# Optimization experiments

Hardware: AMD Instinct MI355X
Metric: run time of the kernel (lower is better)

Reference implementation:

```python
import jax, jax.numpy as jnp
import numpy as np

B, N, L, D_MODEL, H, D_K, D_V = 8, 307, 64, 64, 4, 16, 16


def setup_inputs() -> dict:
    key = jax.random.key(0)
    ks = jax.random.split(key, 10)
    inp = {
        "input_Q": jax.random.normal(ks[0], (B, N, L, D_MODEL), jnp.float32),
        "input_K": jax.random.normal(ks[1], (B, N, L, D_MODEL), jnp.float32),
        "input_V": jax.random.normal(ks[2], (B, N, L, D_MODEL), jnp.float32),
        "attn_mask": jax.random.uniform(ks[3], (B, N, L, 1), jnp.float32),
        "res_att": jax.random.normal(ks[4], (B, N, H, L, L), jnp.float32),
        # Linear weights stored as [in, out] (torch nn.Linear weight transposed)
        "W_Q": jax.random.normal(ks[5], (D_MODEL, H * D_K), jnp.float32) / np.sqrt(D_MODEL),
        "W_K": jax.random.normal(ks[6], (D_MODEL, H * D_K), jnp.float32) / np.sqrt(D_MODEL),
        "W_V": jax.random.normal(ks[7], (D_MODEL, H * D_V), jnp.float32) / np.sqrt(D_MODEL),
        "W_fc": jax.random.normal(ks[8], (H * D_V, D_MODEL), jnp.float32) / np.sqrt(H * D_V),
        # freshly-constructed nn.LayerNorm has weight=1, bias=0
        "ln_scale": jnp.ones((D_MODEL,), jnp.float32),
        "ln_bias": jnp.zeros((D_MODEL,), jnp.float32),
    }
    return inp


def _layernorm(x, scale, bias, eps=1e-5):
    mu = jnp.mean(x, axis=-1, keepdims=True)
    var = jnp.mean(jnp.square(x - mu), axis=-1, keepdims=True)
    return (x - mu) * jax.lax.rsqrt(var + eps) * scale + bias


def reference(input_Q, input_K, input_V, attn_mask, res_att, W_Q, W_K, W_V, W_fc, ln_scale, ln_bias):
    # projections -> [B,N,H,L,d]
    def proj(x, W, d):
        y = jnp.einsum('bnlf,fe->bnle', x, W)
        return y.reshape(B, N, L, H, d).transpose(0, 1, 3, 2, 4)

    Q = proj(input_Q, W_Q, D_K)
    K = proj(input_K, W_K, D_K)
    V = proj(input_V, W_V, D_V)

    # scaled QK^T + residual attention bias: [B,N,H,Lq,Lk]
    scores = jnp.einsum('bnhqd,bnhkd->bnhqk', Q, K) / np.sqrt(D_K) + res_att
    # attn_mask [B,N,L,1] -> broadcast over heads (axis 2) and key dim (last)
    mask = attn_mask[:, :, None, :, :]  # [B,N,1,L,1]
    scores = jnp.where(mask > 0.5, jnp.float32(-1e9), scores)

    # NOTE: original softmaxes over dim=3 (the query axis), faithful here
    attn = jax.nn.softmax(scores, axis=3)
    context = jnp.einsum('bnhqk,bnhkd->bnhqd', attn, V)
    context = context.transpose(0, 1, 3, 2, 4).reshape(B, N, L, H * D_V)
    output = jnp.einsum('bnlc,cf->bnlf', context, W_fc)
    out = _layernorm(output + input_Q, ln_scale, ln_bias)
    return out, scores
```

## Files before the change

kernel.cpp:

```cpp
#include <hip/hip_runtime.h>

#define B_   8
#define N_   307
#define BN   (B_ * N_)
#define OUT_ELEMS (BN * 64 * 64)

typedef float f32x4 __attribute__((ext_vector_type(4)));
typedef short s16x8 __attribute__((ext_vector_type(8)));

__device__ __forceinline__ unsigned short f2bf(float x) {
    unsigned int u = __builtin_bit_cast(unsigned int, x);
    u += 0x7FFFu + ((u >> 16) & 1u);
    return (unsigned short)(u >> 16);
}

__device__ __forceinline__ int swz(int row) { return row ^ ((row >> 3) & 7); }

__device__ __forceinline__ s16x8 ldfrag(const unsigned short* p) {
    return *reinterpret_cast<const s16x8*>(p);
}

__device__ __forceinline__ s16x8 cvt8(float4 lo, float4 hi) {
    s16x8 f;
    f[0] = (short)f2bf(lo.x); f[1] = (short)f2bf(lo.y);
    f[2] = (short)f2bf(lo.z); f[3] = (short)f2bf(lo.w);
    f[4] = (short)f2bf(hi.x); f[5] = (short)f2bf(hi.y);
    f[6] = (short)f2bf(hi.z); f[7] = (short)f2bf(hi.w);
    return f;
}

__device__ __forceinline__ void stage_B(const float* __restrict__ src,
                                        unsigned short* dst, int tid) {
    const float4* s4 = reinterpret_cast<const float4*>(src);
#pragma unroll
    for (int i = 0; i < 4; ++i) {
        int idx = i * 256 + tid;
        float4 v = s4[idx];
        int k  = idx >> 4;
        int n0 = (idx & 15) << 2;
        int ki = k >> 5;
        int qd = (k >> 3) & 3;
        int j  = k & 7;
        float vv[4] = {v.x, v.y, v.z, v.w};
#pragma unroll
        for (int c = 0; c < 4; ++c) {
            int n = n0 + c;
            int row = ((n >> 4) * 2 + ki) * 64 + (qd << 4) + (n & 15);
            dst[(swz(row) << 3) + j] = f2bf(vv[c]);
        }
    }
}

__global__ __launch_bounds__(256, 4) void mta_kernel(
    const float* __restrict__ Xq, const float* __restrict__ Xk,
    const float* __restrict__ Xv, const float* __restrict__ maskp,
    const float* __restrict__ res, const float* __restrict__ Wq,
    const float* __restrict__ Wk, const float* __restrict__ Wv,
    const float* __restrict__ Wfc, const float* __restrict__ lnS,
    const float* __restrict__ lnB, float* __restrict__ out,
    float* __restrict__ scores_out)
{
    __shared__ __align__(16) unsigned char smem[32768];
    unsigned short* sKf = (unsigned short*)(smem);
    unsigned short* sQf = (unsigned short*)(smem + 8192);
    unsigned short* sVf = (unsigned short*)(smem + 16384);
    unsigned short* sWA = (unsigned short*)(smem + 24576);

    const int bn   = blockIdx.x;
    const int tid  = threadIdx.x;
    const int w    = tid >> 6;
    const int lane = tid & 63;
    const int quad = lane >> 4;
    const int l16  = lane & 15;
    const size_t base64 = (size_t)bn * 4096;

    const int toff = (w * 16 + quad * 4) * 64 + l16;

    float4 mv = *reinterpret_cast<const float4*>(maskp + bn * 64 + w * 16 + quad * 4);
    bool bm[4] = {mv.x > 0.5f, mv.y > 0.5f, mv.z > 0.5f, mv.w > 0.5f};

    float rA[4][4], rB[4][4];
    {
        const float* rp = res + (((size_t)(bn * 4)) << 12) + toff;
#pragma unroll
        for (int nt = 0; nt < 4; ++nt)
#pragma unroll
            for (int r = 0; r < 4; ++r)
                rA[nt][r] = rp[r * 64 + nt * 16];
    }

#pragma unroll 1
    for (int pj = 0; pj < 3; ++pj) {
        const float* Xs = (pj == 0) ? Xq : (pj == 1) ? Xk : Xv;
        const float* Ws = (pj == 0) ? Wq : (pj == 1) ? Wk : Wv;
        const float* p = Xs + base64 + (w * 16 + l16) * 64 + quad * 8;
        float4 x0 = *(const float4*)(p);      float4 x1 = *(const float4*)(p + 4);
        float4 x2 = *(const float4*)(p + 32); float4 x3 = *(const float4*)(p + 36);
        stage_B(Ws, sWA, tid);
        __syncthreads();
        s16x8 a0 = cvt8(x0, x1);
        s16x8 a1 = cvt8(x2, x3);
#pragma unroll
        for (int nt = 0; nt < 4; ++nt) {
            f32x4 acc = {0.f, 0.f, 0.f, 0.f};
            s16x8 b0 = ldfrag(sWA + (swz((nt * 2 + 0) * 64 + lane) << 3));
            s16x8 b1 = ldfrag(sWA + (swz((nt * 2 + 1) * 64 + lane) << 3));
            acc = __builtin_amdgcn_mfma_f32_16x16x32_bf16(a0, b0, acc, 0, 0, 0);
            acc = __builtin_amdgcn_mfma_f32_16x16x32_bf16(a1, b1, acc, 0, 0, 0);
            if (pj == 0) {
#pragma unroll
                for (int r = 0; r < 4; ++r) {
                    int rowq = (nt * 4 + w) * 32 + ((l16 >> 3) << 4) + quad * 4 + r;
                    sQf[(swz(rowq) << 3) + (l16 & 7)] = f2bf(acc[r] * 0.25f);
                }
            } else if (pj == 1) {
#pragma unroll
                for (int r = 0; r < 4; ++r) {
                    int rowk = (nt * 4 + w) * 32 + ((l16 >> 3) << 4) + quad * 4 + r;
                    sKf[(swz(rowk) << 3) + (l16 & 7)] = f2bf(acc[r]);
                }
            } else {
#pragma unroll
                for (int r = 0; r < 4; ++r) {
                    int kk = w * 16 + quad * 4 + r;
                    int rowv = (nt * 2 + (kk >> 5)) * 64 + (((kk >> 3) & 3) << 4) + l16;
                    sVf[(swz(rowv) << 3) + (kk & 7)] = f2bf(acc[r]);
                }
            }
        }
        __syncthreads();
    }

    f32x4 ctx[4];
#pragma unroll
    for (int h = 0; h < 4; ++h) ctx[h] = {0.f, 0.f, 0.f, 0.f};

    const s16x8 zf = {0, 0, 0, 0, 0, 0, 0, 0};
#pragma unroll
    for (int h = 0; h < 4; ++h) {
        const size_t sbase = ((size_t)(bn * 4 + h)) << 12;
        float (&rc)[4][4] = (h & 1) ? rB : rA;
        float (&rn)[4][4] = (h & 1) ? rA : rB;
        if (h < 3) {
            const float* rp = res + sbase + 4096 + toff;
#pragma unroll
            for (int nt = 0; nt < 4; ++nt)
#pragma unroll
                for (int r = 0; r < 4; ++r)
                    rn[nt][r] = rp[r * 64 + nt * 16];
        }

        s16x8 aq = zf;
        if (lane < 32) aq = ldfrag(sQf + (swz((h * 4 + w) * 32 + lane) << 3));
        float sv[4][4], Sw[4];
#pragma unroll
        for (int nt = 0; nt < 4; ++nt) {
            s16x8 bk = zf;
            if (lane < 32) bk = ldfrag(sKf + (swz((h * 4 + nt) * 32 + lane) << 3));
            f32x4 t = {0.f, 0.f, 0.f, 0.f};
            t = __builtin_amdgcn_mfma_f32_16x16x32_bf16(aq, bk, t, 0, 0, 0);
#pragma unroll
            for (int r = 0; r < 4; ++r) {
                float s = t[r] + rc[nt][r];
                s = bm[r] ? -1e9f : s;
                scores_out[sbase + toff + r * 64 + nt * 16] = s;
                sv[nt][r] = __expf(s);
            }
            float e = sv[nt][0] + sv[nt][1] + sv[nt][2] + sv[nt][3];
            e += __shfl_xor(e, 16, 64);
            e += __shfl_xor(e, 32, 64);
            Sw[nt] = e;
        }
        float* wS = (h == 0) ? (float*)(smem + 24576) : (float*)(smem + (h - 1) * 2048);
        if (quad == 0) {
#pragma unroll
            for (int nt = 0; nt < 4; ++nt) wS[(nt * 16 + l16) * 4 + w] = Sw[nt];
        }
        __syncthreads();

        float inv[4];
#pragma unroll
        for (int nt = 0; nt < 4; ++nt) {
            float4 vs = *reinterpret_cast<float4*>(&wS[(nt * 16 + l16) * 4]);
            inv[nt] = 1.0f / (vs.x + vs.y + vs.z + vs.w + 1e-30f);
        }
        if (h == 0) __syncthreads();

#pragma unroll
        for (int nt = 0; nt < 4; ++nt) {
            int k  = nt * 16 + l16;
            int rw = (w * 2 + (k >> 5)) * 64 + (((k >> 3) & 3) << 4) + quad * 4;
#pragma unroll
            for (int r = 0; r < 4; ++r)
                sWA[(swz(rw + r) << 3) + (k & 7)] = f2bf(sv[nt][r] * inv[nt]);
        }
        __syncthreads();

#pragma unroll
        for (int ki = 0; ki < 2; ++ki) {
            s16x8 ap = ldfrag(sWA + (swz((w * 2 + ki) * 64 + lane) << 3));
            s16x8 bv = ldfrag(sVf + (swz((h * 2 + ki) * 64 + lane) << 3));
            ctx[h] = __builtin_amdgcn_mfma_f32_16x16x32_bf16(ap, bv, ctx[h], 0, 0, 0);
        }
    }
    __syncthreads();

    float xres[4][4];
    {
        const float* xp = Xq + base64 + toff;
#pragma unroll
        for (int nt = 0; nt < 4; ++nt)
#pragma unroll
            for (int r = 0; r < 4; ++r)
                xres[nt][r] = xp[r * 64 + nt * 16];
    }
#pragma unroll
    for (int hh = 0; hh < 4; ++hh) {
        int c    = hh * 16 + l16;
        int rowb = (w * 2 + (c >> 5)) * 64 + (((c >> 3) & 3) << 4) + quad * 4;
#pragma unroll
        for (int r = 0; r < 4; ++r)
            sQf[(swz(rowb + r) << 3) + (c & 7)] = f2bf(ctx[hh][r]);
    }
    stage_B(Wfc, sWA, tid);
    __syncthreads();

    f32x4 oacc[4];
    {
        s16x8 a0 = ldfrag(sQf + (swz((w * 2 + 0) * 64 + lane) << 3));
        s16x8 a1 = ldfrag(sQf + (swz((w * 2 + 1) * 64 + lane) << 3));
#pragma unroll
        for (int nt = 0; nt < 4; ++nt) {
            f32x4 acc = {0.f, 0.f, 0.f, 0.f};
            s16x8 b0 = ldfrag(sWA + (swz((nt * 2 + 0) * 64 + lane) << 3));
            s16x8 b1 = ldfrag(sWA + (swz((nt * 2 + 1) * 64 + lane) << 3));
            acc = __builtin_amdgcn_mfma_f32_16x16x32_bf16(a0, b0, acc, 0, 0, 0);
            acc = __builtin_amdgcn_mfma_f32_16x16x32_bf16(a1, b1, acc, 0, 0, 0);
            oacc[nt] = acc;
        }
    }

    float scl[4], bia[4];
#pragma unroll
    for (int nt = 0; nt < 4; ++nt) {
        scl[nt] = lnS[nt * 16 + l16];
        bia[nt] = lnB[nt * 16 + l16];
    }
#pragma unroll
    for (int r = 0; r < 4; ++r) {
        float px[4], sum = 0.f, sq = 0.f;
#pragma unroll
        for (int nt = 0; nt < 4; ++nt) {
            float x = oacc[nt][r] + xres[nt][r];
            px[nt] = x; sum += x; sq += x * x;
        }
#pragma unroll
        for (int m = 1; m <= 8; m <<= 1) {
            sum += __shfl_xor(sum, m, 64);
            sq  += __shfl_xor(sq,  m, 64);
        }
        float mu   = sum * 0.015625f;
        float var  = sq * 0.015625f - mu * mu;
        float rstd = rsqrtf(var + 1e-5f);
#pragma unroll
        for (int nt = 0; nt < 4; ++nt) {
            out[base64 + toff + r * 64 + nt * 16] = (px[nt] - mu) * rstd * scl[nt] + bia[nt];
        }
    }
}

extern "C" void kernel_launch(void* const* d_in, const int* in_sizes, int n_in,
                              void* d_out, int out_size, void* d_ws, size_t ws_size,
                              hipStream_t stream) {
    const float* Xq   = (const float*)d_in[0];
    const float* Xk   = (const float*)d_in[1];
    const float* Xv   = (const float*)d_in[2];
    const float* msk  = (const float*)d_in[3];
    const float* res  = (const float*)d_in[4];
    const float* Wq   = (const float*)d_in[5];
    const float* Wk   = (const float*)d_in[6];
    const float* Wv   = (const float*)d_in[7];
    const float* Wfc  = (const float*)d_in[8];
    const float* lnS  = (const float*)d_in[9];
    const float* lnB  = (const float*)d_in[10];
    float* out    = (float*)d_out;
    float* scores = out + OUT_ELEMS;
    mta_kernel<<<BN, 256, 0, stream>>>(Xq, Xk, Xv, msk, res, Wq, Wk, Wv, Wfc,
                                       lnS, lnB, out, scores);
}
```

Before: 100.0 us.

## Assign one head per wave so softmax over queries needs no block sync

Attention work is redistributed so each of the four waves owns one head and computes the full 64x64 score tile for it. The query-axis softmax sum then stays inside a wave, using shuffles instead of shared-memory partial sums and several block barriers per head. The residual bias is loaded straight into the MFMA accumulators with double-buffered prefetch, and the Wfc staging is issued earlier. In exchange each wave holds more registers (eight accumulator tiles), which may lower occupancy, and it reuses the K/Q shared buffers as scratch for the probability tiles.

Result: slower. 121.3 us (+21.3%).

```diff
diff --git a/kernel.cpp b/kernel.cpp
--- a/kernel.cpp
+++ b/kernel.cpp
@@ -74,21 +74,6 @@
     const int l16  = lane & 15;
     const size_t base64 = (size_t)bn * 4096;
 
-    const int toff = (w * 16 + quad * 4) * 64 + l16;
-
-    float4 mv = *reinterpret_cast<const float4*>(maskp + bn * 64 + w * 16 + quad * 4);
-    bool bm[4] = {mv.x > 0.5f, mv.y > 0.5f, mv.z > 0.5f, mv.w > 0.5f};
-
-    float rA[4][4], rB[4][4];
-    {
-        const float* rp = res + (((size_t)(bn * 4)) << 12) + toff;
-#pragma unroll
-        for (int nt = 0; nt < 4; ++nt)
-#pragma unroll
-            for (int r = 0; r < 4; ++r)
-                rA[nt][r] = rp[r * 64 + nt * 16];
-    }
-
 #pragma unroll 1
     for (int pj = 0; pj < 3; ++pj) {
         const float* Xs = (pj == 0) ? Xq : (pj == 1) ? Xk : Xv;
@@ -131,80 +116,103 @@
         __syncthreads();
     }
 
+    stage_B(Wfc, sWA, tid);
+
+    const int h = w;
+    const size_t sbase = ((size_t)(bn * 4 + h)) << 12;
+
+    unsigned mbits = 0u;
+#pragma unroll
+    for (int mt = 0; mt < 4; ++mt) {
+        float4 mv = *reinterpret_cast<const float4*>(maskp + bn * 64 + mt * 16 + quad * 4);
+        mbits |= (mv.x > 0.5f ? 1u : 0u) << (mt * 4 + 0);
+        mbits |= (mv.y > 0.5f ? 1u : 0u) << (mt * 4 + 1);
+        mbits |= (mv.z > 0.5f ? 1u : 0u) << (mt * 4 + 2);
+        mbits |= (mv.w > 0.5f ? 1u : 0u) << (mt * 4 + 3);
+    }
+
+    const s16x8 zf = {0, 0, 0, 0, 0, 0, 0, 0};
+    s16x8 aq[4], bk[4];
+#pragma unroll
+    for (int t = 0; t < 4; ++t) {
+        aq[t] = (lane < 32) ? ldfrag(sQf + (swz((h * 4 + t) * 32 + lane) << 3)) : zf;
+        bk[t] = (lane < 32) ? ldfrag(sKf + (swz((h * 4 + t) * 32 + lane) << 3)) : zf;
+    }
+    unsigned short* scrA = sKf + w * 1024;
+    unsigned short* scrB = sQf + w * 1024;
+
+    const float* rp = res + sbase + quad * 256 + l16;
+    float*       sp = scores_out + sbase + quad * 256 + l16;
+
     f32x4 ctx[4];
 #pragma unroll
-    for (int h = 0; h < 4; ++h) ctx[h] = {0.f, 0.f, 0.f, 0.f};
-
-    const s16x8 zf = {0, 0, 0, 0, 0, 0, 0, 0};
-#pragma unroll
-    for (int h = 0; h < 4; ++h) {
-        const size_t sbase = ((size_t)(bn * 4 + h)) << 12;
-        float (&rc)[4][4] = (h & 1) ? rB : rA;
-        float (&rn)[4][4] = (h & 1) ? rA : rB;
-        if (h < 3) {
-            const float* rp = res + sbase + 4096 + toff;
-#pragma unroll
-            for (int nt = 0; nt < 4; ++nt)
+    for (int mt = 0; mt < 4; ++mt) ctx[mt] = {0.f, 0.f, 0.f, 0.f};
+
+    f32x4 acc[2][4];
+#pragma unroll
+    for (int mt = 0; mt < 4; ++mt)
+#pragma unroll
+        for (int r = 0; r < 4; ++r)
+            acc[0][mt][r] = rp[mt * 1024 + r * 64];
+
+#pragma unroll
+    for (int nt = 0; nt < 4; ++nt) {
+        const int cb = nt & 1, nb = cb ^ 1;
+#pragma unroll
+        for (int mt = 0; mt < 4; ++mt)
+            acc[cb][mt] = __builtin_amdgcn_mfma_f32_16x16x32_bf16(aq[mt], bk[nt], acc[cb][mt], 0, 0, 0);
+        if (nt < 3) {
+#pragma unroll
+            for (int mt = 0; mt < 4; ++mt)
 #pragma unroll
                 for (int r = 0; r < 4; ++r)
-                    rn[nt][r] = rp[r * 64 + nt * 16];
-        }
-
-        s16x8 aq = zf;
-        if (lane < 32) aq = ldfrag(sQf + (swz((h * 4 + w) * 32 + lane) << 3));
-        float sv[4][4], Sw[4];
-#pragma unroll
-        for (int nt = 0; nt < 4; ++nt) {
-            s16x8 bk = zf;
-            if (lane < 32) bk = ldfrag(sKf + (swz((h * 4 + nt) * 32 + lane) << 3));
-            f32x4 t = {0.f, 0.f, 0.f, 0.f};
-            t = __builtin_amdgcn_mfma_f32_16x16x32_bf16(aq, bk, t, 0, 0, 0);
+                    acc[nb][mt][r] = rp[mt * 1024 + r * 64 + (nt + 1) * 16];
+        }
+        float esum = 0.f;
+#pragma unroll
+        for (int mt = 0; mt < 4; ++mt)
 #pragma unroll
             for (int r = 0; r < 4; ++r) {
-                float s = t[r] + rc[nt][r];
-                s = bm[r] ? -1e9f : s;
-                scores_out[sbase + toff + r * 64 + nt * 16] = s;
-                sv[nt][r] = __expf(s);
+                float s = acc[cb][mt][r];
+                s = ((mbits >> (mt * 4 + r)) & 1u) ? -1e9f : s;
+                sp[mt * 1024 + r * 64 + nt * 16] = s;
+                float e = __expf(s);
+                acc[cb][mt][r] = e;
+                esum += e;
             }
-            float e = sv[nt][0] + sv[nt][1] + sv[nt][2] + sv[nt][3];
-            e += __shfl_xor(e, 16, 64);
-            e += __shfl_xor(e, 32, 64);
-            Sw[nt] = e;
-        }
-        float* wS = (h == 0) ? (float*)(smem + 24576) : (float*)(smem + (h - 1) * 2048);
-        if (quad == 0) {
-#pragma unroll
-            for (int nt = 0; nt < 4; ++nt) wS[(nt * 16 + l16) * 4 + w] = Sw[nt];
-        }
-        __syncthreads();
-
-        float inv[4];
-#pragma unroll
-        for (int nt = 0; nt < 4; ++nt) {
-            float4 vs = *reinterpret_cast<float4*>(&wS[(nt * 16 + l16) * 4]);
-            inv[nt] = 1.0f / (vs.x + vs.y + vs.z + vs.w + 1e-30f);
-        }
-        if (h == 0) __syncthreads();
-
-#pragma unroll
-        for (int nt = 0; nt < 4; ++nt) {
-            int k  = nt * 16 + l16;
-            int rw = (w * 2 + (k >> 5)) * 64 + (((k >> 3) & 3) << 4) + quad * 4;
+        esum += __shfl_xor(esum, 16, 64);
+        esum += __shfl_xor(esum, 32, 64);
+        float inv = 1.0f / (esum + 1e-30f);
+#pragma unroll
+        for (int mt = 0; mt < 4; ++mt) {
+            unsigned short* scr = ((mt < 2) ? scrA : scrB) + (mt & 1) * 512;
+            int rl = (((nt * 2 + (l16 >> 3)) & 3) << 4) + quad * 4;
 #pragma unroll
             for (int r = 0; r < 4; ++r)
-                sWA[(swz(rw + r) << 3) + (k & 7)] = f2bf(sv[nt][r] * inv[nt]);
-        }
-        __syncthreads();
-
-#pragma unroll
-        for (int ki = 0; ki < 2; ++ki) {
-            s16x8 ap = ldfrag(sWA + (swz((w * 2 + ki) * 64 + lane) << 3));
+                scr[(swz(rl + r) << 3) + (l16 & 7)] = f2bf(acc[cb][mt][r] * inv);
+        }
+        if (cb == 1) {
+            const int ki = nt >> 1;
             s16x8 bv = ldfrag(sVf + (swz((h * 2 + ki) * 64 + lane) << 3));
-            ctx[h] = __builtin_amdgcn_mfma_f32_16x16x32_bf16(ap, bv, ctx[h], 0, 0, 0);
-        }
-    }
+#pragma unroll
+            for (int mt = 0; mt < 4; ++mt) {
+                s16x8 ap = ldfrag(((mt < 2) ? scrA : scrB) + (mt & 1) * 512 + (swz(lane) << 3));
+                ctx[mt] = __builtin_amdgcn_mfma_f32_16x16x32_bf16(ap, bv, ctx[mt], 0, 0, 0);
+            }
+        }
+    }
+
     __syncthreads();
 
+#pragma unroll
+    for (int mt = 0; mt < 4; ++mt) {
+        int c    = h * 16 + l16;
+        int rowb = (mt * 2 + (c >> 5)) * 64 + (((c >> 3) & 3) << 4) + quad * 4;
+#pragma unroll
+        for (int r = 0; r < 4; ++r)
+            sQf[(swz(rowb + r) << 3) + (c & 7)] = f2bf(ctx[mt][r]);
+    }
+    const int toff = (w * 16 + quad * 4) * 64 + l16;
     float xres[4][4];
     {
         const float* xp = Xq + base64 + toff;
@@ -214,15 +222,12 @@
             for (int r = 0; r < 4; ++r)
                 xres[nt][r] = xp[r * 64 + nt * 16];
     }
-#pragma unroll
-    for (int hh = 0; hh < 4; ++hh) {
-        int c    = hh * 16 + l16;
-        int rowb = (w * 2 + (c >> 5)) * 64 + (((c >> 3) & 3) << 4) + quad * 4;
-#pragma unroll
-        for (int r = 0; r < 4; ++r)
-            sQf[(swz(rowb + r) << 3) + (c & 7)] = f2bf(ctx[hh][r]);
-    }
-    stage_B(Wfc, sWA, tid);
+    float scl[4], bia[4];
+#pragma unroll
+    for (int nt = 0; nt < 4; ++nt) {
+        scl[nt] = lnS[nt * 16 + l16];
+        bia[nt] = lnB[nt * 16 + l16];
+    }
     __syncthreads();
 
     f32x4 oacc[4];
@@ -231,21 +236,15 @@
         s16x8 a1 = ldfrag(sQf + (swz((w * 2 + 1) * 64 + lane) << 3));
 #pragma unroll
         for (int nt = 0; nt < 4; ++nt) {
-            f32x4 acc = {0.f, 0.f, 0.f, 0.f};
+            f32x4 a = {0.f, 0.f, 0.f, 0.f};
             s16x8 b0 = ldfrag(sWA + (swz((nt * 2 + 0) * 64 + lane) << 3));
             s16x8 b1 = ldfrag(sWA + (swz((nt * 2 + 1) * 64 + lane) << 3));
-            acc = __builtin_amdgcn_mfma_f32_16x16x32_bf16(a0, b0, acc, 0, 0, 0);
-            acc = __builtin_amdgcn_mfma_f32_16x16x32_bf16(a1, b1, acc, 0, 0, 0);
-            oacc[nt] = acc;
-        }
-    }
-
-    float scl[4], bia[4];
-#pragma unroll
-    for (int nt = 0; nt < 4; ++nt) {
-        scl[nt] = lnS[nt * 16 + l16];
-        bia[nt] = lnB[nt * 16 + l16];
-    }
+            a = __builtin_amdgcn_mfma_f32_16x16x32_bf16(a0, b0, a, 0, 0, 0);
+            a = __builtin_amdgcn_mfma_f32_16x16x32_bf16(a1, b1, a, 0, 0, 0);
+            oacc[nt] = a;
+        }
+    }
+
 #pragma unroll
     for (int r = 0; r < 4; ++r) {
         float px[4], sum = 0.f, sq = 0.f;
```

## Keep Q in registers via transposed MFMA, shrink LDS, fold residual into accumulator

Applied to the files above, without the earlier changes.

Computes the Q projection with swapped MFMA operands so the packed bf16 Q fragments stay in registers and are redistributed with shuffles, which removes the 8KB Q shared buffer. Shared memory drops to 24KB and the launch bound rises to 6 blocks per CU to raise occupancy. The residual attention bias is passed in as the MFMA accumulator, one barrier inside the head loop is removed, and the Xq residual and LayerNorm parameter loads are moved into the last head iteration. The higher block target risks register spills, and removing the barrier between the sWA probability writes and the cross-wave reads may introduce a race.

Measured after the change: 249.2 us. +149.2%, slower.

```diff
diff --git a/kernel.cpp b/kernel.cpp
--- a/kernel.cpp
+++ b/kernel.cpp
@@ -7,6 +7,7 @@
 
 typedef float f32x4 __attribute__((ext_vector_type(4)));
 typedef short s16x8 __attribute__((ext_vector_type(8)));
+typedef unsigned int u32x4 __attribute__((ext_vector_type(4)));
 
 __device__ __forceinline__ unsigned short f2bf(float x) {
     unsigned int u = __builtin_bit_cast(unsigned int, x);
@@ -51,7 +52,7 @@
     }
 }
 
-__global__ __launch_bounds__(256, 4) void mta_kernel(
+__global__ __launch_bounds__(256, 6) void mta_kernel(
     const float* __restrict__ Xq, const float* __restrict__ Xk,
     const float* __restrict__ Xv, const float* __restrict__ maskp,
     const float* __restrict__ res, const float* __restrict__ Wq,
@@ -60,11 +61,10 @@
     const float* __restrict__ lnB, float* __restrict__ out,
     float* __restrict__ scores_out)
 {
-    __shared__ __align__(16) unsigned char smem[32768];
+    __shared__ __align__(16) unsigned char smem[24576];
     unsigned short* sKf = (unsigned short*)(smem);
-    unsigned short* sQf = (unsigned short*)(smem + 8192);
-    unsigned short* sVf = (unsigned short*)(smem + 16384);
-    unsigned short* sWA = (unsigned short*)(smem + 24576);
+    unsigned short* sVf = (unsigned short*)(smem + 8192);
+    unsigned short* sWA = (unsigned short*)(smem + 16384);
 
     const int bn   = blockIdx.x;
     const int tid  = threadIdx.x;
@@ -88,6 +88,8 @@
             for (int r = 0; r < 4; ++r)
                 rA[nt][r] = rp[r * 64 + nt * 16];
     }
+
+    unsigned qpk[4][2];
 
 #pragma unroll 1
     for (int pj = 0; pj < 3; ++pj) {
@@ -105,26 +107,29 @@
             f32x4 acc = {0.f, 0.f, 0.f, 0.f};
             s16x8 b0 = ldfrag(sWA + (swz((nt * 2 + 0) * 64 + lane) << 3));
             s16x8 b1 = ldfrag(sWA + (swz((nt * 2 + 1) * 64 + lane) << 3));
-            acc = __builtin_amdgcn_mfma_f32_16x16x32_bf16(a0, b0, acc, 0, 0, 0);
-            acc = __builtin_amdgcn_mfma_f32_16x16x32_bf16(a1, b1, acc, 0, 0, 0);
             if (pj == 0) {
-#pragma unroll
-                for (int r = 0; r < 4; ++r) {
-                    int rowq = (nt * 4 + w) * 32 + ((l16 >> 3) << 4) + quad * 4 + r;
-                    sQf[(swz(rowq) << 3) + (l16 & 7)] = f2bf(acc[r] * 0.25f);
-                }
-            } else if (pj == 1) {
-#pragma unroll
-                for (int r = 0; r < 4; ++r) {
-                    int rowk = (nt * 4 + w) * 32 + ((l16 >> 3) << 4) + quad * 4 + r;
-                    sKf[(swz(rowk) << 3) + (l16 & 7)] = f2bf(acc[r]);
-                }
+                acc = __builtin_amdgcn_mfma_f32_16x16x32_bf16(b0, a0, acc, 0, 0, 0);
+                acc = __builtin_amdgcn_mfma_f32_16x16x32_bf16(b1, a1, acc, 0, 0, 0);
+                qpk[nt][0] = (unsigned)f2bf(acc[0] * 0.25f)
+                           | ((unsigned)f2bf(acc[1] * 0.25f) << 16);
+                qpk[nt][1] = (unsigned)f2bf(acc[2] * 0.25f)
+                           | ((unsigned)f2bf(acc[3] * 0.25f) << 16);
             } else {
-#pragma unroll
-                for (int r = 0; r < 4; ++r) {
-                    int kk = w * 16 + quad * 4 + r;
-                    int rowv = (nt * 2 + (kk >> 5)) * 64 + (((kk >> 3) & 3) << 4) + l16;
-                    sVf[(swz(rowv) << 3) + (kk & 7)] = f2bf(acc[r]);
+                acc = __builtin_amdgcn_mfma_f32_16x16x32_bf16(a0, b0, acc, 0, 0, 0);
+                acc = __builtin_amdgcn_mfma_f32_16x16x32_bf16(a1, b1, acc, 0, 0, 0);
+                if (pj == 1) {
+#pragma unroll
+                    for (int r = 0; r < 4; ++r) {
+                        int rowk = (nt * 4 + w) * 32 + ((l16 >> 3) << 4) + quad * 4 + r;
+                        sKf[(swz(rowk) << 3) + (l16 & 7)] = f2bf(acc[r]);
+                    }
+                } else {
+#pragma unroll
+                    for (int r = 0; r < 4; ++r) {
+                        int kk = w * 16 + quad * 4 + r;
+                        int rowv = (nt * 2 + (kk >> 5)) * 64 + (((kk >> 3) & 3) << 4) + l16;
+                        sVf[(swz(rowv) << 3) + (kk & 7)] = f2bf(acc[r]);
+                    }
                 }
             }
         }
@@ -134,6 +139,8 @@
     f32x4 ctx[4];
 #pragma unroll
     for (int h = 0; h < 4; ++h) ctx[h] = {0.f, 0.f, 0.f, 0.f};
+
+    float xres[4][4], scl[4], bia[4];
 
     const s16x8 zf = {0, 0, 0, 0, 0, 0, 0, 0};
 #pragma unroll
@@ -148,21 +155,39 @@
 #pragma unroll
                 for (int r = 0; r < 4; ++r)
                     rn[nt][r] = rp[r * 64 + nt * 16];
-        }
-
-        s16x8 aq = zf;
-        if (lane < 32) aq = ldfrag(sQf + (swz((h * 4 + w) * 32 + lane) << 3));
+        } else {
+            const float* xp = Xq + base64 + toff;
+#pragma unroll
+            for (int nt = 0; nt < 4; ++nt) {
+#pragma unroll
+                for (int r = 0; r < 4; ++r) xres[nt][r] = xp[r * 64 + nt * 16];
+                scl[nt] = lnS[nt * 16 + l16];
+                bia[nt] = lnB[nt * 16 + l16];
+            }
+        }
+
+        s16x8 aq;
+        {
+            int p0 = ((lane & 16) << 1) + l16;
+            unsigned w0 = __shfl(qpk[h][0], p0, 64);
+            unsigned w1 = __shfl(qpk[h][1], p0, 64);
+            unsigned w2 = __shfl(qpk[h][0], p0 + 16, 64);
+            unsigned w3 = __shfl(qpk[h][1], p0 + 16, 64);
+            if (lane >= 32) { w0 = 0; w1 = 0; w2 = 0; w3 = 0; }
+            u32x4 uv = {w0, w1, w2, w3};
+            aq = __builtin_bit_cast(s16x8, uv);
+        }
+
         float sv[4][4], Sw[4];
 #pragma unroll
         for (int nt = 0; nt < 4; ++nt) {
             s16x8 bk = zf;
             if (lane < 32) bk = ldfrag(sKf + (swz((h * 4 + nt) * 32 + lane) << 3));
-            f32x4 t = {0.f, 0.f, 0.f, 0.f};
-            t = __builtin_amdgcn_mfma_f32_16x16x32_bf16(aq, bk, t, 0, 0, 0);
+            f32x4 cin = {rc[nt][0], rc[nt][1], rc[nt][2], rc[nt][3]};
+            f32x4 t = __builtin_amdgcn_mfma_f32_16x16x32_bf16(aq, bk, cin, 0, 0, 0);
 #pragma unroll
             for (int r = 0; r < 4; ++r) {
-                float s = t[r] + rc[nt][r];
-                s = bm[r] ? -1e9f : s;
+                float s = bm[r] ? -1e9f : t[r];
                 scores_out[sbase + toff + r * 64 + nt * 16] = s;
                 sv[nt][r] = __expf(s);
             }
@@ -171,7 +196,7 @@
             e += __shfl_xor(e, 32, 64);
             Sw[nt] = e;
         }
-        float* wS = (h == 0) ? (float*)(smem + 24576) : (float*)(smem + (h - 1) * 2048);
+        float* wS = (h == 0) ? (float*)(smem + 16384) : (float*)(smem + (h - 1) * 2048);
         if (quad == 0) {
 #pragma unroll
             for (int nt = 0; nt < 4; ++nt) wS[(nt * 16 + l16) * 4 + w] = Sw[nt];
@@ -182,7 +207,7 @@
 #pragma unroll
         for (int nt = 0; nt < 4; ++nt) {
             float4 vs = *reinterpret_cast<float4*>(&wS[(nt * 16 + l16) * 4]);
-            inv[nt] = 1.0f / (vs.x + vs.y + vs.z + vs.w + 1e-30f);
+            inv[nt] = 1.0f / (vs.x + vs.y + vs.z + vs.w);
         }
         if (h == 0) __syncthreads();
 
@@ -194,8 +219,6 @@
             for (int r = 0; r < 4; ++r)
                 sWA[(swz(rw + r) << 3) + (k & 7)] = f2bf(sv[nt][r] * inv[nt]);
         }
-        __syncthreads();
-
 #pragma unroll
         for (int ki = 0; ki < 2; ++ki) {
             s16x8 ap = ldfrag(sWA + (swz((w * 2 + ki) * 64 + lane) << 3));
@@ -205,47 +228,32 @@
     }
     __syncthreads();
 
-    float xres[4][4];
-    {
-        const float* xp = Xq + base64 + toff;
-#pragma unroll
-        for (int nt = 0; nt < 4; ++nt)
-#pragma unroll
-            for (int r = 0; r < 4; ++r)
-                xres[nt][r] = xp[r * 64 + nt * 16];
-    }
 #pragma unroll
     for (int hh = 0; hh < 4; ++hh) {
         int c    = hh * 16 + l16;
         int rowb = (w * 2 + (c >> 5)) * 64 + (((c >> 3) & 3) << 4) + quad * 4;
 #pragma unroll
         for (int r = 0; r < 4; ++r)
-            sQf[(swz(rowb + r) << 3) + (c & 7)] = f2bf(ctx[hh][r]);
+            sKf[(swz(rowb + r) << 3) + (c & 7)] = f2bf(ctx[hh][r]);
     }
     stage_B(Wfc, sWA, tid);
     __syncthreads();
 
     f32x4 oacc[4];
     {
-        s16x8 a0 = ldfrag(sQf + (swz((w * 2 + 0) * 64 + lane) << 3));
-        s16x8 a1 = ldfrag(sQf + (swz((w * 2 + 1) * 64 + lane) << 3));
-#pragma unroll
-        for (int nt = 0; nt < 4; ++nt) {
-            f32x4 acc = {0.f, 0.f, 0.f, 0.f};
+        s16x8 a0 = ldfrag(sKf + (swz((w * 2 + 0) * 64 + lane) << 3));
+        s16x8 a1 = ldfrag(sKf + (swz((w * 2 + 1) * 64 + lane) << 3));
+#pragma unroll
+        for (int nt = 0; nt < 4; ++nt) {
+            f32x4 a = {0.f, 0.f, 0.f, 0.f};
             s16x8 b0 = ldfrag(sWA + (swz((nt * 2 + 0) * 64 + lane) << 3));
             s16x8 b1 = ldfrag(sWA + (swz((nt * 2 + 1) * 64 + lane) << 3));
-            acc = __builtin_amdgcn_mfma_f32_16x16x32_bf16(a0, b0, acc, 0, 0, 0);
-            acc = __builtin_amdgcn_mfma_f32_16x16x32_bf16(a1, b1, acc, 0, 0, 0);
-            oacc[nt] = acc;
-        }
-    }
-
-    float scl[4], bia[4];
-#pragma unroll
-    for (int nt = 0; nt < 4; ++nt) {
-        scl[nt] = lnS[nt * 16 + l16];
-        bia[nt] = lnB[nt * 16 + l16];
-    }
+            a = __builtin_amdgcn_mfma_f32_16x16x32_bf16(a0, b0, a, 0, 0, 0);
+            a = __builtin_amdgcn_mfma_f32_16x16x32_bf16(a1, b1, a, 0, 0, 0);
+            oacc[nt] = a;
+        }
+    }
+
 #pragma unroll
     for (int r = 0; r < 4; ++r) {
         float px[4], sum = 0.f, sq = 0.f;
```

## Transpose score tiles so softmax reduces in-wave and use double-buffered P

Applied to the files above, without the earlier changes.

Swaps the MFMA operands for QK^T so each wave holds full query columns for its keys. The query-axis softmax sum then reduces with intra-wave shuffles instead of a cross-wave shared-memory exchange and an extra barrier. The residual bias is fed as the MFMA accumulator, and res and score accesses become contiguous 16-byte vector loads and stores. The probability tile is double-buffered across heads to drop a barrier, at the cost of 8KB more LDS per block and recomputing exp twice.

Result: slower. 103.1 us (+3.1%).

```diff
diff --git a/kernel.cpp b/kernel.cpp
--- a/kernel.cpp
+++ b/kernel.cpp
@@ -60,11 +60,12 @@
     const float* __restrict__ lnB, float* __restrict__ out,
     float* __restrict__ scores_out)
 {
-    __shared__ __align__(16) unsigned char smem[32768];
+    __shared__ __align__(16) unsigned char smem[40960];
     unsigned short* sKf = (unsigned short*)(smem);
     unsigned short* sQf = (unsigned short*)(smem + 8192);
     unsigned short* sVf = (unsigned short*)(smem + 16384);
-    unsigned short* sWA = (unsigned short*)(smem + 24576);
+    unsigned short* sW0 = (unsigned short*)(smem + 24576);
+    unsigned short* sW1 = (unsigned short*)(smem + 32768);
 
     const int bn   = blockIdx.x;
     const int tid  = threadIdx.x;
@@ -74,19 +75,19 @@
     const int l16  = lane & 15;
     const size_t base64 = (size_t)bn * 4096;
 
-    const int toff = (w * 16 + quad * 4) * 64 + l16;
-
-    float4 mv = *reinterpret_cast<const float4*>(maskp + bn * 64 + w * 16 + quad * 4);
-    bool bm[4] = {mv.x > 0.5f, mv.y > 0.5f, mv.z > 0.5f, mv.w > 0.5f};
-
-    float rA[4][4], rB[4][4];
+    const int soff0 = l16 * 64 + w * 16 + quad * 4;
+
+    bool bmv[4];
+#pragma unroll
+    for (int nt = 0; nt < 4; ++nt)
+        bmv[nt] = maskp[bn * 64 + nt * 16 + l16] > 0.5f;
+
+    f32x4 rA[4];
     {
-        const float* rp = res + (((size_t)(bn * 4)) << 12) + toff;
+        const float* rp = res + (((size_t)(bn * 4)) << 12) + soff0;
 #pragma unroll
         for (int nt = 0; nt < 4; ++nt)
-#pragma unroll
-            for (int r = 0; r < 4; ++r)
-                rA[nt][r] = rp[r * 64 + nt * 16];
+            rA[nt] = *reinterpret_cast<const f32x4*>(rp + nt * 1024);
     }
 
 #pragma unroll 1
@@ -96,15 +97,15 @@
         const float* p = Xs + base64 + (w * 16 + l16) * 64 + quad * 8;
         float4 x0 = *(const float4*)(p);      float4 x1 = *(const float4*)(p + 4);
         float4 x2 = *(const float4*)(p + 32); float4 x3 = *(const float4*)(p + 36);
-        stage_B(Ws, sWA, tid);
+        stage_B(Ws, sW0, tid);
         __syncthreads();
         s16x8 a0 = cvt8(x0, x1);
         s16x8 a1 = cvt8(x2, x3);
 #pragma unroll
         for (int nt = 0; nt < 4; ++nt) {
             f32x4 acc = {0.f, 0.f, 0.f, 0.f};
-            s16x8 b0 = ldfrag(sWA + (swz((nt * 2 + 0) * 64 + lane) << 3));
-            s16x8 b1 = ldfrag(sWA + (swz((nt * 2 + 1) * 64 + lane) << 3));
+            s16x8 b0 = ldfrag(sW0 + (swz((nt * 2 + 0) * 64 + lane) << 3));
+            s16x8 b1 = ldfrag(sW0 + (swz((nt * 2 + 1) * 64 + lane) << 3));
             acc = __builtin_amdgcn_mfma_f32_16x16x32_bf16(a0, b0, acc, 0, 0, 0);
             acc = __builtin_amdgcn_mfma_f32_16x16x32_bf16(a1, b1, acc, 0, 0, 0);
             if (pj == 0) {
@@ -139,80 +140,76 @@
 #pragma unroll
     for (int h = 0; h < 4; ++h) {
         const size_t sbase = ((size_t)(bn * 4 + h)) << 12;
-        float (&rc)[4][4] = (h & 1) ? rB : rA;
-        float (&rn)[4][4] = (h & 1) ? rA : rB;
+        unsigned short* buf = (h & 1) ? sW1 : sW0;
+
+        s16x8 bk = zf;
+        if (lane < 32) bk = ldfrag(sKf + (swz((h * 4 + w) * 32 + lane) << 3));
+
+        f32x4 sr[4];
+        float esum[4] = {0.f, 0.f, 0.f, 0.f};
+#pragma unroll
+        for (int nt = 0; nt < 4; ++nt) {
+            s16x8 aq = zf;
+            if (lane < 32) aq = ldfrag(sQf + (swz((h * 4 + nt) * 32 + lane) << 3));
+            f32x4 t = __builtin_amdgcn_mfma_f32_16x16x32_bf16(bk, aq, rA[nt], 0, 0, 0);
+#pragma unroll
+            for (int r = 0; r < 4; ++r) {
+                float s = bmv[nt] ? -1e9f : t[r];
+                sr[nt][r] = s;
+                esum[r] += __expf(s);
+            }
+        }
+#pragma unroll
+        for (int m = 1; m <= 8; m <<= 1)
+#pragma unroll
+            for (int r = 0; r < 4; ++r)
+                esum[r] += __shfl_xor(esum[r], m, 64);
+        float inv[4];
+#pragma unroll
+        for (int r = 0; r < 4; ++r) inv[r] = 1.0f / (esum[r] + 1e-30f);
+
+#pragma unroll
+        for (int nt = 0; nt < 4; ++nt) {
+            int row = (nt * 2 + (w >> 1)) * 64 + (((w & 1) << 1) + (quad >> 1)) * 16 + l16;
+            short4 pk;
+            pk.x = (short)f2bf(__expf(sr[nt][0]) * inv[0]);
+            pk.y = (short)f2bf(__expf(sr[nt][1]) * inv[1]);
+            pk.z = (short)f2bf(__expf(sr[nt][2]) * inv[2]);
+            pk.w = (short)f2bf(__expf(sr[nt][3]) * inv[3]);
+            *reinterpret_cast<short4*>(buf + (swz(row) << 3) + ((quad & 1) << 2)) = pk;
+        }
+        __syncthreads();
+
         if (h < 3) {
-            const float* rp = res + sbase + 4096 + toff;
+            const float* rp2 = res + sbase + 4096 + soff0;
 #pragma unroll
             for (int nt = 0; nt < 4; ++nt)
-#pragma unroll
-                for (int r = 0; r < 4; ++r)
-                    rn[nt][r] = rp[r * 64 + nt * 16];
-        }
-
-        s16x8 aq = zf;
-        if (lane < 32) aq = ldfrag(sQf + (swz((h * 4 + w) * 32 + lane) << 3));
-        float sv[4][4], Sw[4];
-#pragma unroll
-        for (int nt = 0; nt < 4; ++nt) {
-            s16x8 bk = zf;
-            if (lane < 32) bk = ldfrag(sKf + (swz((h * 4 + nt) * 32 + lane) << 3));
-            f32x4 t = {0.f, 0.f, 0.f, 0.f};
-            t = __builtin_amdgcn_mfma_f32_16x16x32_bf16(aq, bk, t, 0, 0, 0);
-#pragma unroll
-            for (int r = 0; r < 4; ++r) {
-                float s = t[r] + rc[nt][r];
-                s = bm[r] ? -1e9f : s;
-                scores_out[sbase + toff + r * 64 + nt * 16] = s;
-                sv[nt][r] = __expf(s);
-            }
-            float e = sv[nt][0] + sv[nt][1] + sv[nt][2] + sv[nt][3];
-            e += __shfl_xor(e, 16, 64);
-            e += __shfl_xor(e, 32, 64);
-            Sw[nt] = e;
-        }
-        float* wS = (h == 0) ? (float*)(smem + 24576) : (float*)(smem + (h - 1) * 2048);
-        if (quad == 0) {
-#pragma unroll
-            for (int nt = 0; nt < 4; ++nt) wS[(nt * 16 + l16) * 4 + w] = Sw[nt];
-        }
-        __syncthreads();
-
-        float inv[4];
-#pragma unroll
-        for (int nt = 0; nt < 4; ++nt) {
-            float4 vs = *reinterpret_cast<float4*>(&wS[(nt * 16 + l16) * 4]);
-            inv[nt] = 1.0f / (vs.x + vs.y + vs.z + vs.w + 1e-30f);
-        }
-        if (h == 0) __syncthreads();
-
-#pragma unroll
-        for (int nt = 0; nt < 4; ++nt) {
-            int k  = nt * 16 + l16;
-            int rw = (w * 2 + (k >> 5)) * 64 + (((k >> 3) & 3) << 4) + quad * 4;
-#pragma unroll
-            for (int r = 0; r < 4; ++r)
-                sWA[(swz(rw + r) << 3) + (k & 7)] = f2bf(sv[nt][r] * inv[nt]);
-        }
-        __syncthreads();
+                rA[nt] = *reinterpret_cast<const f32x4*>(rp2 + nt * 1024);
+        }
+#pragma unroll
+        for (int nt = 0; nt < 4; ++nt)
+            *reinterpret_cast<f32x4*>(scores_out + sbase + soff0 + nt * 1024) = sr[nt];
 
 #pragma unroll
         for (int ki = 0; ki < 2; ++ki) {
-            s16x8 ap = ldfrag(sWA + (swz((w * 2 + ki) * 64 + lane) << 3));
+            s16x8 ap = ldfrag(buf + (swz((w * 2 + ki) * 64 + lane) << 3));
             s16x8 bv = ldfrag(sVf + (swz((h * 2 + ki) * 64 + lane) << 3));
             ctx[h] = __builtin_amdgcn_mfma_f32_16x16x32_bf16(ap, bv, ctx[h], 0, 0, 0);
         }
     }
     __syncthreads();
 
-    float xres[4][4];
+    const int toff = (w * 16 + quad * 4) * 64 + l16;
+    float xres[4][4], scl[4], bia[4];
     {
         const float* xp = Xq + base64 + toff;
 #pragma unroll
-        for (int nt = 0; nt < 4; ++nt)
-#pragma unroll
-            for (int r = 0; r < 4; ++r)
-                xres[nt][r] = xp[r * 64 + nt * 16];
+        for (int nt = 0; nt < 4; ++nt) {
+#pragma unroll
+            for (int r = 0; r < 4; ++r) xres[nt][r] = xp[r * 64 + nt * 16];
+            scl[nt] = lnS[nt * 16 + l16];
+            bia[nt] = lnB[nt * 16 + l16];
+        }
     }
 #pragma unroll
     for (int hh = 0; hh < 4; ++hh) {
@@ -220,32 +217,26 @@
         int rowb = (w * 2 + (c >> 5)) * 64 + (((c >> 3) & 3) << 4) + quad * 4;
 #pragma unroll
         for (int r = 0; r < 4; ++r)
-            sQf[(swz(rowb + r) << 3) + (c & 7)] = f2bf(ctx[hh][r]);
-    }
-    stage_B(Wfc, sWA, tid);
+            sKf[(swz(rowb + r) << 3) + (c & 7)] = f2bf(ctx[hh][r]);
+    }
+    stage_B(Wfc, sW0, tid);
     __syncthreads();
 
     f32x4 oacc[4];
     {
-        s16x8 a0 = ldfrag(sQf + (swz((w * 2 + 0) * 64 + lane) << 3));
-        s16x8 a1 = ldfrag(sQf + (swz((w * 2 + 1) * 64 + lane) << 3));
-#pragma unroll
-        for (int nt = 0; nt < 4; ++nt) {
-            f32x4 acc = {0.f, 0.f, 0.f, 0.f};
-            s16x8 b0 = ldfrag(sWA + (swz((nt * 2 + 0) * 64 + lane) << 3));
-            s16x8 b1 = ldfrag(sWA + (swz((nt * 2 + 1) * 64 + lane) << 3));
-            acc = __builtin_amdgcn_mfma_f32_16x16x32_bf16(a0, b0, acc, 0, 0, 0);
-            acc = __builtin_amdgcn_mfma_f32_16x16x32_bf16(a1, b1, acc, 0, 0, 0);
-            oacc[nt] = acc;
-        }
-    }
-
-    float scl[4], bia[4];
-#pragma unroll
-    for (int nt = 0; nt < 4; ++nt) {
-        scl[nt] = lnS[nt * 16 + l16];
-        bia[nt] = lnB[nt * 16 + l16];
-    }
+        s16x8 a0 = ldfrag(sKf + (swz((w * 2 + 0) * 64 + lane) << 3));
+        s16x8 a1 = ldfrag(sKf + (swz((w * 2 + 1) * 64 + lane) << 3));
+#pragma unroll
+        for (int nt = 0; nt < 4; ++nt) {
+            f32x4 a = {0.f, 0.f, 0.f, 0.f};
+            s16x8 b0 = ldfrag(sW0 + (swz((nt * 2 + 0) * 64 + lane) << 3));
+            s16x8 b1 = ldfrag(sW0 + (swz((nt * 2 + 1) * 64 + lane) << 3));
+            a = __builtin_amdgcn_mfma_f32_16x16x32_bf16(a0, b0, a, 0, 0, 0);
+            a = __builtin_amdgcn_mfma_f32_16x16x32_bf16(a1, b1, a, 0, 0, 0);
+            oacc[nt] = a;
+        }
+    }
+
 #pragma unroll
     for (int r = 0; r < 4; ++r) {
         float px[4], sum = 0.f, sq = 0.f;
```
